# Optimization experiments

Hardware: AMD Instinct MI355X
Metric: run time of the kernel (lower is better)

Reference implementation:

```python
import jax, jax.numpy as jnp
import numpy as np

# constants from init_kwargs (data_info / model_cfg)
FX = 300.0
FY = 300.0
CX = 128.0
CY = 128.0
BG = 1.0            # data_info['bg_color']
EPS2D = 0.3         # gsplat screen-space blur added to 2D covariance diagonal
NEAR = 0.01         # gsplat near-plane cull
C0 = 0.28209479177387814  # SH degree-0 basis
N_PTS = 512
IMG = 256


def quat_to_rotmat(q):
    # q: (N,4) wxyz, normalized inside
    q = q / jnp.linalg.norm(q, axis=-1, keepdims=True)
    w, x, y, z = q[:, 0], q[:, 1], q[:, 2], q[:, 3]
    return jnp.stack([
        jnp.stack([1 - 2 * (y * y + z * z), 2 * (x * y - w * z), 2 * (x * z + w * y)], -1),
        jnp.stack([2 * (x * y + w * z), 1 - 2 * (x * x + z * z), 2 * (y * z - w * x)], -1),
        jnp.stack([2 * (x * z - w * y), 2 * (y * z + w * x), 1 - 2 * (x * x + y * y)], -1),
    ], axis=-2)  # (N,3,3)


def setup_inputs() -> dict:
    key = jax.random.key(0)
    k = jax.random.split(key, 6)
    means = (jax.random.uniform(k[0], (N_PTS, 3), dtype=jnp.float32) - 0.5) * 10.0
    quats = jax.random.normal(k[1], (N_PTS, 4), dtype=jnp.float32)
    # log-scales around 0.2m so Gaussians actually cover pixels
    scales = jnp.log(0.2) + 0.1 * jax.random.normal(k[2], (N_PTS, 3), dtype=jnp.float32)
    opacities = jax.random.normal(k[3], (N_PTS,), dtype=jnp.float32)
    sh0 = 0.5 * jax.random.normal(k[4], (N_PTS, 1, 3), dtype=jnp.float32)
    shN = 0.01 * jax.random.normal(k[5], (N_PTS, 15, 3), dtype=jnp.float32)
    camtoworld = jnp.concatenate([jnp.eye(3, dtype=jnp.float32), jnp.zeros((3, 1), jnp.float32)], axis=1)
    return {"camtoworld": camtoworld, "means": means, "quats": quats, "scales": scales,
            "opacities": opacities, "sh0": sh0, "shN": shN, "img_h": IMG, "img_w": IMG}


def _render(camtoworld, means, quats, scales, opacities, sh0, shN, img_h, img_w):
    # --- camera setup (matches module forward) ---
    c2w = jnp.eye(4, dtype=jnp.float32).at[:3, :].set(camtoworld)
    viewmat = jnp.linalg.inv(c2w)
    viewmat = viewmat.at[1, :].multiply(-1.0).at[2, :].multiply(-1.0)
    R, t = viewmat[:3, :3], viewmat[:3, 3]

    # --- project means ---
    p = means @ R.T + t                      # (N,3) camera-space
    x, y, z = p[:, 0], p[:, 1], p[:, 2]
    valid = z > NEAR
    zs = jnp.where(valid, z, 1.0)
    rz = 1.0 / zs

    # --- 3D covariance: R(q) diag(s^2) R(q)^T, rotated to camera ---
    Rq = quat_to_rotmat(quats)
    M = Rq * jnp.exp(scales)[:, None, :]
    cov3d = M @ jnp.swapaxes(M, 1, 2)        # (N,3,3)
    cov_cam = jnp.einsum('ij,njk,lk->nil', R, cov3d, R)

    # --- EWA perspective Jacobian with fov clipping (gsplat persp_proj) ---
    limx = 1.3 * (0.5 * img_w / FX)
    limy = 1.3 * (0.5 * img_h / FY)
    tx = zs * jnp.clip(x * rz, -limx, limx)
    ty = zs * jnp.clip(y * rz, -limy, limy)
    zero = jnp.zeros_like(rz)
    J = jnp.stack([
        jnp.stack([FX * rz, zero, -FX * tx * rz * rz], -1),
        jnp.stack([zero, FY * rz, -FY * ty * rz * rz], -1),
    ], axis=1)                               # (N,2,3)
    cov2d = jnp.einsum('nij,njk,nlk->nil', J, cov_cam, J)
    a = cov2d[:, 0, 0] + EPS2D
    b = cov2d[:, 0, 1]
    c = cov2d[:, 1, 1] + EPS2D
    det = a * c - b * b
    valid = valid & (det > 1e-12)
    dets = jnp.where(valid, det, 1.0)
    cA, cB, cC = c / dets, -b / dets, a / dets   # conic (inverse 2D covariance)

    mx = FX * x * rz + CX
    my = FY * y * rz + CY

    # --- colors: sh_degree = 0 -> only sh0 band, clamped to >= 0 ---
    color = jnp.maximum(C0 * sh0[:, 0, :] + 0.5, 0.0)   # (N,3)
    opac = jax.nn.sigmoid(opacities)

    # --- depth sort (front to back) ---
    order = jnp.argsort(jnp.where(valid, z, jnp.inf))
    mx, my, cA, cB, cC, opac, color, valid = (v[order] for v in (mx, my, cA, cB, cC, opac, color, valid))

    # --- per-pixel alpha evaluation (dense [N,H,W]) ---
    px = jnp.arange(img_w, dtype=jnp.float32) + 0.5
    py = jnp.arange(img_h, dtype=jnp.float32) + 0.5
    dx = px[None, None, :] - mx[:, None, None]          # (N,H,W)
    dy = py[None, :, None] - my[:, None, None]
    sigma = 0.5 * (cA[:, None, None] * dx * dx + cC[:, None, None] * dy * dy) + cB[:, None, None] * dx * dy
    alpha = jnp.minimum(0.999, opac[:, None, None] * jnp.exp(-sigma))
    alpha = jnp.where((sigma >= 0.0) & (alpha >= 1.0 / 255.0) & valid[:, None, None], alpha, 0.0)

    # --- front-to-back alpha compositing via exclusive cumprod of (1-alpha) ---
    T = jnp.cumprod(1.0 - alpha, axis=0)                # (N,H,W)
    T_excl = jnp.concatenate([jnp.ones_like(T[:1]), T[:-1]], axis=0)
    w = T_excl * alpha
    render = jnp.einsum('nhw,nc->hwc', w, color) + T[-1][..., None] * BG   # (H,W,3)
    alpha_map = (1.0 - T[-1])[..., None]                                   # (H,W,1)
    return render, alpha_map


def reference(camtoworld, means, quats, scales, opacities, sh0, shN, img_h, img_w):
    return _render(camtoworld, means, quats, scales, opacities, sh0, shN, img_h, img_w)
```

## Files before the change

### kernel.cpp

```cpp
#include <hip/hip_runtime.h>
#include <math.h>

#define FXc 300.0f
#define FYc 300.0f
#define CXc 128.0f
#define CYc 128.0f
#define BGc 1.0f
#define EPS2Dc 0.3f
#define NEARc 0.01f
#define C0c 0.28209479177387814f

#define MAXP 512
#define SEG  8

typedef float v2f __attribute__((ext_vector_type(2)));

__global__ void __launch_bounds__(1024)
gs_fused(const float* __restrict__ cam,
         const float* __restrict__ means,
         const float* __restrict__ quats,
         const float* __restrict__ scales,
         const float* __restrict__ opacs,
         const float* __restrict__ sh0,
         const int* __restrict__ img_w_p,
         float* __restrict__ out,
         int n, int npix)
{
    __shared__ float4 spts[MAXP][2];
    __shared__ __align__(16) float zc[MAXP + 4];
    __shared__ int scnt[MAXP / 64];
    __shared__ int sbase[MAXP / 64 + 1];
    __shared__ float4 comb[SEG - 1][256];

    const int lt   = threadIdx.x;
    const int wave = lt >> 6;

    const int W = *img_w_p;
    const int tiles_x = W >> 4;
    const int tx = (blockIdx.x % tiles_x) << 4;
    const int ty = (blockIdx.x / tiles_x) << 4;
    const float tx0 = (float)tx + 0.5f, tx1 = (float)tx + 15.5f;
    const float ty0 = (float)ty + 0.5f, ty1 = (float)ty + 15.5f;

    const int nchunks = (n + 63) >> 6;

    float pmx = 0.f, pmy = 0.f, pA_ = 0.f, pB_ = 0.f, pC_ = 0.f;
    float pop = 0.f, pcr = 0.f, pcg = 0.f, pcb = 0.f, pz = 0.f;
    unsigned long long mreg = 0ull;
    bool phit = false;

    if (lt < MAXP) {
        const float a00 = cam[0], a01 = cam[1], a02 = cam[2],  b0 = cam[3];
        const float a10 = cam[4], a11 = cam[5], a12 = cam[6],  b1 = cam[7];
        const float a20 = cam[8], a21 = cam[9], a22 = cam[10], b2 = cam[11];
        const float det3 = a00*(a11*a22 - a12*a21) - a01*(a10*a22 - a12*a20) + a02*(a10*a21 - a11*a20);
        const float id = 1.0f / det3;
        const float i00 = (a11*a22 - a12*a21)*id, i01 = (a02*a21 - a01*a22)*id, i02 = (a01*a12 - a02*a11)*id;
        const float i10 = (a12*a20 - a10*a22)*id, i11 = (a00*a22 - a02*a20)*id, i12 = (a02*a10 - a00*a12)*id;
        const float i20 = (a10*a21 - a11*a20)*id, i21 = (a01*a20 - a00*a21)*id, i22 = (a00*a11 - a01*a10)*id;
        const float R00 = i00,  R01 = i01,  R02 = i02;
        const float R10 = -i10, R11 = -i11, R12 = -i12;
        const float R20 = -i20, R21 = -i21, R22 = -i22;
        const float t0 = -(i00*b0 + i01*b1 + i02*b2);
        const float t1 = (i10*b0 + i11*b1 + i12*b2);
        const float t2 = (i20*b0 + i21*b1 + i22*b2);
        const float limx_e = 1.3f * (0.5f * (float)W / FXc);
        const float limy_e = limx_e;

        const int p = lt;
        bool hit = false;
        if (p < n) {
            const float m0 = means[3*p], m1 = means[3*p+1], m2 = means[3*p+2];
            const float px_ = R00*m0 + R01*m1 + R02*m2 + t0;
            const float py_ = R10*m0 + R11*m1 + R12*m2 + t1;
            const float pz_ = R20*m0 + R21*m1 + R22*m2 + t2;

            bool valid = pz_ > NEARc;
            const float zs = valid ? pz_ : 1.0f;
            const float rz = 1.0f / zs;

            float qw = quats[4*p], qx = quats[4*p+1], qy = quats[4*p+2], qz = quats[4*p+3];
            const float qn = rsqrtf(qw*qw + qx*qx + qy*qy + qz*qz);
            qw *= qn; qx *= qn; qy *= qn; qz *= qn;
            const float Rq00 = 1.f - 2.f*(qy*qy + qz*qz), Rq01 = 2.f*(qx*qy - qw*qz), Rq02 = 2.f*(qx*qz + qw*qy);
            const float Rq10 = 2.f*(qx*qy + qw*qz), Rq11 = 1.f - 2.f*(qx*qx + qz*qz), Rq12 = 2.f*(qy*qz - qw*qx);
            const float Rq20 = 2.f*(qx*qz - qw*qy), Rq21 = 2.f*(qy*qz + qw*qx), Rq22 = 1.f - 2.f*(qx*qx + qy*qy);

            const float e0 = __expf(scales[3*p]), e1 = __expf(scales[3*p+1]), e2 = __expf(scales[3*p+2]);
            const float M00 = Rq00*e0, M01 = Rq01*e1, M02 = Rq02*e2;
            const float M10 = Rq10*e0, M11 = Rq11*e1, M12 = Rq12*e2;
            const float M20 = Rq20*e0, M21 = Rq21*e1, M22 = Rq22*e2;

            const float S00 = M00*M00 + M01*M01 + M02*M02;
            const float S01 = M00*M10 + M01*M11 + M02*M12;
            const float S02 = M00*M20 + M01*M21 + M02*M22;
            const float S11 = M10*M10 + M11*M11 + M12*M12;
            const float S12 = M10*M20 + M11*M21 + M12*M22;
            const float S22 = M20*M20 + M21*M21 + M22*M22;

            const float U00 = R00*S00 + R01*S01 + R02*S02;
            const float U01 = R00*S01 + R01*S11 + R02*S12;
            const float U02 = R00*S02 + R01*S12 + R02*S22;
            const float U10 = R10*S00 + R11*S01 + R12*S02;
            const float U11 = R10*S01 + R11*S11 + R12*S12;
            const float U12 = R10*S02 + R11*S12 + R12*S22;
            const float U20 = R20*S00 + R21*S01 + R22*S02;
            const float U21 = R20*S01 + R21*S11 + R22*S12;
            const float U22 = R20*S02 + R21*S12 + R22*S22;

            const float C00 = U00*R00 + U01*R01 + U02*R02;
            const float C01 = U00*R10 + U01*R11 + U02*R12;
            const float C02 = U00*R20 + U01*R21 + U02*R22;
            const float C11 = U10*R10 + U11*R11 + U12*R12;
            const float C12 = U10*R20 + U11*R21 + U12*R22;
            const float C22 = U20*R20 + U21*R21 + U22*R22;

            const float txc = zs * fminf(fmaxf(px_*rz, -limx_e), limx_e);
            const float tyc = zs * fminf(fmaxf(py_*rz, -limy_e), limy_e);
            const float ja0 = FXc * rz;
            const float ja2 = -FXc * txc * rz * rz;
            const float jb1 = FYc * rz;
            const float jb2 = -FYc * tyc * rz * rz;

            const float c2d00 = ja0*ja0*C00 + 2.f*ja0*ja2*C02 + ja2*ja2*C22 + EPS2Dc;
            const float c2d01 = ja0*jb1*C01 + ja0*jb2*C02 + ja2*jb1*C12 + ja2*jb2*C22;
            const float c2d11 = jb1*jb1*C11 + 2.f*jb1*jb2*C12 + jb2*jb2*C22 + EPS2Dc;

            const float det2 = c2d00*c2d11 - c2d01*c2d01;
            valid = valid && (det2 > 1e-12f);
            const float rdet = 1.0f / (valid ? det2 : 1.0f);
            pA_ = c2d11 * rdet;
            pB_ = -c2d01 * rdet;
            pC_ = c2d00 * rdet;

            pmx = FXc * px_ * rz + CXc;
            pmy = FYc * py_ * rz + CYc;

            pcr = fmaxf(C0c * sh0[3*p+0] + 0.5f, 0.0f);
            pcg = fmaxf(C0c * sh0[3*p+1] + 0.5f, 0.0f);
            pcb = fmaxf(C0c * sh0[3*p+2] + 0.5f, 0.0f);
            pop = 1.0f / (1.0f + __expf(-opacs[p]));
            pz  = pz_;

            if (valid) {
                const float a_ = pA_, b_ = pB_, c_ = pC_;
                const float dx0 = tx0 - pmx, dx1 = tx1 - pmx;
                const float dy0 = ty0 - pmy, dy1 = ty1 - pmy;
                float smin;
                if (dx0 <= 0.f && 0.f <= dx1 && dy0 <= 0.f && 0.f <= dy1) {
                    smin = 0.f;
                } else {
                    const float ra = 1.0f / a_, rc = 1.0f / c_;
                    float yy = fminf(fmaxf(-b_ * dx0 * rc, dy0), dy1);
                    float s0 = 0.5f*a_*dx0*dx0 + b_*dx0*yy + 0.5f*c_*yy*yy;
                    yy = fminf(fmaxf(-b_ * dx1 * rc, dy0), dy1);
                    float s1 = 0.5f*a_*dx1*dx1 + b_*dx1*yy + 0.5f*c_*yy*yy;
                    float xx = fminf(fmaxf(-b_ * dy0 * ra, dx0), dx1);
                    float s2 = 0.5f*a_*xx*xx + b_*xx*dy0 + 0.5f*c_*dy0*dy0;
                    xx = fminf(fmaxf(-b_ * dy1 * ra, dx0), dx1);
                    float s3 = 0.5f*a_*xx*xx + b_*xx*dy1 + 0.5f*c_*dy1*dy1;
                    smin = fminf(fminf(s0, s1), fminf(s2, s3));
                }
                hit = (smin <= __logf(pop * 255.0f) + 1e-3f);
            }
        }
        phit = hit;
        mreg = __ballot(hit);
        if ((lt & 63) == 0) scnt[wave] = __popcll(mreg);
    }
    __syncthreads();

    if (lt == 0) {
        int acc = 0;
        for (int c = 0; c < nchunks; ++c) { sbase[c] = acc; acc += scnt[c]; }
        sbase[nchunks] = acc;
    }
    __syncthreads();
    const int k = sbase[nchunks];

    int pslot = -1;
    if (lt < MAXP && phit) {
        pslot = sbase[wave] + __popcll(mreg & ((1ull << (lt & 63)) - 1ull));
        zc[pslot] = pz;
    }
    if (lt < 4) zc[k + lt] = INFINITY;
    __syncthreads();

    if (pslot >= 0) {
        const float za = pz;
        const int sa = pslot;
        int rank = 0;
        const float4* z4 = (const float4*)zc;
        const int k4 = (k + 3) >> 2;
        for (int j4 = 0; j4 < k4; ++j4) {
            const float4 v = z4[j4];
            const int j = j4 << 2;
            rank += (v.x < za || (v.x == za && (j+0) < sa));
            rank += (v.y < za || (v.y == za && (j+1) < sa));
            rank += (v.z < za || (v.z == za && (j+2) < sa));
            rank += (v.w < za || (v.w == za && (j+3) < sa));
        }
        unsigned ur = __float_as_uint(pcr);
        ur = (ur + 0x7FFFu + ((ur >> 16) & 1u)) & 0xFFFF0000u;
        unsigned ug = __float_as_uint(pcg);
        ug = (ug + 0x7FFFu + ((ug >> 16) & 1u)) >> 16;
        const float crcg = __uint_as_float(ur | ug);
        spts[rank][0] = make_float4(pmx, pmy, 0.5f * pA_, pB_);
        spts[rank][1] = make_float4(0.5f * pC_, pop, crcg, pcb);
    }
    __syncthreads();

    const int s  = lt >> 7;
    const int p0 = lt & 127;
    const int col  = tx + (p0 & 15);
    const int row0 = ty + (p0 >> 4);
    const float px  = (float)col + 0.5f;
    const float py0 = (float)row0 + 0.5f;

    const int beg = (k * s) >> 3;
    const int end = (k * (s + 1)) >> 3;

    const v2f pyv = {py0, py0 + 8.0f};
    v2f T = {1.0f, 1.0f};
    v2f Rv = {0.f, 0.f}, Gv = {0.f, 0.f}, Bv = {0.f, 0.f};

    for (int base = beg; base < end; base += 4) {
        const int lim = (base + 4 < end) ? base + 4 : end;
        #pragma unroll 4
        for (int i = base; i < lim; ++i) {
            const float4 a4 = spts[i][0];
            const float4 b4 = spts[i][1];

            const float dx = px - a4.x;
            const v2f dy = pyv - a4.y;
            const float u = a4.z * dx * dx;
            const v2f tt = b4.x * dy + a4.w * dx;
            const v2f sg = dy * tt + u;

            const v2f e = {__expf(-sg.x), __expf(-sg.y)};
            v2f al = b4.y * e;
            al.x = fminf(al.x, 0.999f);
            al.y = fminf(al.y, 0.999f);
            al.x = ((sg.x >= 0.0f) && (al.x >= (1.0f/255.0f))) ? al.x : 0.0f;
            al.y = ((sg.y >= 0.0f) && (al.y >= (1.0f/255.0f))) ? al.y : 0.0f;

            const unsigned uc = __float_as_uint(b4.z);
            const float crf = __uint_as_float(uc & 0xFFFF0000u);
            const float cgf = __uint_as_float(uc << 16);

            const v2f w = T * al;
            Rv += w * crf;
            Gv += w * cgf;
            Bv += w * b4.w;
            T  -= al * T;
        }
        if (!__any(fmaxf(T.x, T.y) > 1e-4f)) break;
    }

    if (s > 0) {
        comb[s - 1][p0]       = make_float4(Rv.x, Gv.x, Bv.x, T.x);
        comb[s - 1][p0 + 128] = make_float4(Rv.y, Gv.y, Bv.y, T.y);
    }
    __syncthreads();

    if (s == 0) {
        float rr = Rv.x, gg = Gv.x, bb = Bv.x, Tt = T.x;
        #pragma unroll
        for (int ss = 0; ss < SEG - 1; ++ss) {
            const float4 f = comb[ss][p0];
            rr += Tt * f.x; gg += Tt * f.y; bb += Tt * f.z; Tt *= f.w;
        }
        rr += Tt * BGc; gg += Tt * BGc; bb += Tt * BGc;
        int opix = row0 * W + col;
        out[3*opix + 0] = rr;
        out[3*opix + 1] = gg;
        out[3*opix + 2] = bb;
        out[3*npix + opix] = 1.0f - Tt;

        rr = Rv.y; gg = Gv.y; bb = Bv.y; Tt = T.y;
        #pragma unroll
        for (int ss = 0; ss < SEG - 1; ++ss) {
            const float4 f = comb[ss][p0 + 128];
            rr += Tt * f.x; gg += Tt * f.y; bb += Tt * f.z; Tt *= f.w;
        }
        rr += Tt * BGc; gg += Tt * BGc; bb += Tt * BGc;
        opix = (row0 + 8) * W + col;
        out[3*opix + 0] = rr;
        out[3*opix + 1] = gg;
        out[3*opix + 2] = bb;
        out[3*npix + opix] = 1.0f - Tt;
    }
}

extern "C" void kernel_launch(void* const* d_in, const int* in_sizes, int n_in,
                              void* d_out, int out_size, void* d_ws, size_t ws_size,
                              hipStream_t stream) {
    const float* cam    = (const float*)d_in[0];
    const float* means  = (const float*)d_in[1];
    const float* quats  = (const float*)d_in[2];
    const float* scales = (const float*)d_in[3];
    const float* opacs  = (const float*)d_in[4];
    const float* sh0    = (const float*)d_in[5];
    const int* img_w = (const int*)d_in[8];

    const int n = in_sizes[4];
    const int npix = out_size / 4;

    const int blocks = npix / 256;
    gs_fused<<<blocks, 1024, 0, stream>>>(cam, means, quats, scales, opacs, sh0,
                                          img_w, (float*)d_out, n, npix);
}
```

Before: 10.52 us.

## Truncate per-tile gaussian list once guaranteed transmittance falls below threshold

For each gaussian it computes a lower bound on alpha over the 16x16 tile, using the largest sigma at the tile corners, and stores log(1-alpha_min). After depth sorting, a block-wide prefix sum over these values finds the first gaussian at which every pixel's transmittance is guaranteed to be tiny, and compositing stops there. This saves blending work for occluded gaussians but adds a scan, a ballot, an atomic and extra syncs. It also changes the output slightly, since dropped contributions with T below about 2e-5 are no longer added.

```diff
diff --git a/kernel.cpp b/kernel.cpp
--- a/kernel.cpp
+++ b/kernel.cpp
@@ -28,6 +28,9 @@
 {
     __shared__ float4 spts[MAXP][2];
     __shared__ __align__(16) float zc[MAXP + 4];
+    __shared__ float carr[MAXP];
+    __shared__ float wtot[8];
+    __shared__ int   skcut;
     __shared__ int scnt[MAXP / 64];
     __shared__ int sbase[MAXP / 64 + 1];
     __shared__ float4 comb[SEG - 1][256];
@@ -46,6 +49,7 @@
 
     float pmx = 0.f, pmy = 0.f, pA_ = 0.f, pB_ = 0.f, pC_ = 0.f;
     float pop = 0.f, pcr = 0.f, pcg = 0.f, pcb = 0.f, pz = 0.f;
+    float pcf = 0.f;
     unsigned long long mreg = 0ull;
     bool phit = false;
 
@@ -162,6 +166,15 @@
                     smin = fminf(fminf(s0, s1), fminf(s2, s3));
                 }
                 hit = (smin <= __logf(pop * 255.0f) + 1e-3f);
+
+                const float q00 = 0.5f*(a_*dx0*dx0 + c_*dy0*dy0) + b_*dx0*dy0;
+                const float q01 = 0.5f*(a_*dx0*dx0 + c_*dy1*dy1) + b_*dx0*dy1;
+                const float q10 = 0.5f*(a_*dx1*dx1 + c_*dy0*dy0) + b_*dx1*dy0;
+                const float q11 = 0.5f*(a_*dx1*dx1 + c_*dy1*dy1) + b_*dx1*dy1;
+                const float smax = fmaxf(fmaxf(q00, q01), fmaxf(q10, q11));
+                const float amin = pop * __expf(-smax);
+                pcf = (hit && amin >= 1.05f/255.0f)
+                    ? __logf(1.0f - fminf(amin, 0.999f)) : 0.0f;
             }
         }
         phit = hit;
@@ -174,6 +187,7 @@
         int acc = 0;
         for (int c = 0; c < nchunks; ++c) { sbase[c] = acc; acc += scnt[c]; }
         sbase[nchunks] = acc;
+        skcut = MAXP;
     }
     __syncthreads();
     const int k = sbase[nchunks];
@@ -207,8 +221,37 @@
         const float crcg = __uint_as_float(ur | ug);
         spts[rank][0] = make_float4(pmx, pmy, 0.5f * pA_, pB_);
         spts[rank][1] = make_float4(0.5f * pC_, pop, crcg, pcb);
-    }
-    __syncthreads();
+        carr[rank] = pcf;
+    }
+    __syncthreads();
+
+    float v = 0.f;
+    if (lt < MAXP) {
+        v = (lt < k) ? carr[lt] : 0.0f;
+        #pragma unroll
+        for (int d = 1; d < 64; d <<= 1) {
+            const float t = __shfl_up(v, d, 64);
+            if ((lt & 63) >= d) v += t;
+        }
+        if ((lt & 63) == 63) wtot[wave] = v;
+    }
+    __syncthreads();
+    {
+        float p = 0.f;
+        if (lt < MAXP) {
+            float off = 0.f;
+            for (int j = 0; j < wave; ++j) off += wtot[j];
+            p = off + v;
+        }
+        const bool cross = (lt < MAXP) && (lt < k) && (p < -10.82f);
+        const unsigned long long bm = __ballot(cross);
+        if (bm && (lt & 63) == 0) {
+            const int cand = (wave << 6) + (__ffsll((unsigned long long)bm) - 1) + 1;
+            atomicMin(&skcut, cand);
+        }
+    }
+    __syncthreads();
+    const int kc = (k < skcut) ? k : skcut;
 
     const int s  = lt >> 7;
     const int p0 = lt & 127;
@@ -217,8 +260,8 @@
     const float px  = (float)col + 0.5f;
     const float py0 = (float)row0 + 0.5f;
 
-    const int beg = (k * s) >> 3;
-    const int end = (k * (s + 1)) >> 3;
+    const int beg = (kc * s) >> 3;
+    const int end = (kc * (s + 1)) >> 3;
 
     const v2f pyv = {py0, py0 + 8.0f};
     v2f T = {1.0f, 1.0f};
```

Result: slower. 11.43 us (+8.6%).
